# Kernel optimization log

Hardware: AMD Instinct MI355X
Metric: run time of the kernel (lower is better)

Reference implementation:

```python
import jax, jax.numpy as jnp
import numpy as np

B, N, C, P = 16, 4096, 4, 64
D = 128        # conv output channels (fixed in module)
WIN = 7        # window_size
ALPHA = 0.5
EPS = 1e-5     # BatchNorm eps


def setup_inputs() -> dict:
    key = jax.random.key(0)
    k1, k2, k3, k4 = jax.random.split(key, 4)
    x = jax.random.normal(k1, (B, N, C, P), jnp.float32)
    x_template = jax.random.normal(k2, (B, N, C, P), jnp.float32)
    # Conv1d(n_channel, 128, kernel_size=n_pts): weight [128, C, P], bias [128]
    W = jax.random.normal(k3, (D, C, P), jnp.float32) * 0.05
    b = jax.random.normal(k4, (D,), jnp.float32) * 0.01
    gamma = jnp.ones((D,), jnp.float32)   # BN weight init = 1
    beta = jnp.zeros((D,), jnp.float32)   # BN bias init = 0
    return {"x": x, "x_template": x_template, "W": W, "b": b, "gamma": gamma, "beta": beta}


def _embed(x_flat, W, b, gamma, beta):
    # Conv1d with kernel_size == full length -> contraction over (C, P), output length 1.
    h = jnp.einsum('ncp,dcp->nd', x_flat, W) + b           # [B*N, D]
    # BatchNorm1d in training mode: per-channel stats over the (B*N, L=1) batch.
    mean = h.mean(axis=0)
    var = h.var(axis=0)                                     # biased variance (torch BN)
    h = (h - mean) / jnp.sqrt(var + EPS) * gamma + beta
    return jnp.where(h >= 0, h, 0.1 * h)                    # LeakyReLU(0.1)


def reference(x, x_template, W, b, gamma, beta):
    nb, nc, ch, npt = x.shape
    hw = WIN // 2
    off = jnp.arange(-hw, hw + 1)
    raw = jnp.arange(nc)[:, None] + off[None, :]
    valid = (raw >= 0) & (raw < nc)                         # dedups clamped edge cols (matches dense mask)
    cols = jnp.clip(raw, 0, nc - 1)

    emb_x = _embed(x.reshape(nb * nc, ch, npt), W, b, gamma, beta).reshape(nb, nc, D)
    emb_t = _embed(x_template.reshape(nb * nc, ch, npt), W, b, gamma, beta).reshape(nb, nc, D)

    # Banded similarity: only the window entries the module actually uses.
    emb_t_win = emb_t[:, cols]
    sim = jnp.einsum('bnd,bnwd->bnw', emb_x, emb_t_win)

    # feat_fused = raw sim gathered at clamped window inds (duplicates at edges kept)
    feat_fused = sim

    # Masked softmax over the window (invalid = clamped duplicates excluded, as in dense mask)
    mx = jnp.where(valid, sim, -jnp.inf).max(axis=-1, keepdims=True)
    e = jnp.where(valid, jnp.exp(sim - mx), 0.0)
    attn = e / e.sum(axis=-1, keepdims=True)

    xt_flat = x_template.reshape(nb, nc, ch * npt)
    out = jnp.einsum('bnw,bnwe->bne', attn, xt_flat[:, cols])  # [B, N, C*P]
    out = out.reshape(nb, nc, ch, npt)
    out = ALPHA * x + (1.0 - ALPHA) * out
    return out, feat_fused
```

## Files before the change

### kernel.cpp

```cpp
#include <hip/hip_runtime.h>
#include <math.h>

#define BB 16
#define NN 4096
#define DD 128
#define KK 256
#define NROWS (BB*NN)
#define WIN 7
#define HWIN 3
#define ALPHA 0.5f
#define EPS 1e-5f

typedef __attribute__((ext_vector_type(8))) short bf16x8;
typedef __attribute__((ext_vector_type(4))) float f32x4;

__device__ __forceinline__ unsigned short f2b(float f) {
    unsigned u = __float_as_uint(f);
    u += 0x7FFFu + ((u >> 16) & 1u);
    return (unsigned short)(u >> 16);
}
__device__ __forceinline__ float b2f_lo(unsigned v) { return __uint_as_float(v << 16); }
__device__ __forceinline__ float b2f_hi(unsigned v) { return __uint_as_float(v & 0xFFFF0000u); }
__device__ __forceinline__ float lrelu(float v) { return v >= 0.f ? v : 0.1f * v; }

__device__ __forceinline__ uint4 pack8(float4 a, float4 b) {
    uint4 v;
    v.x = (unsigned)f2b(a.x)  | ((unsigned)f2b(a.y)  << 16);
    v.y = (unsigned)f2b(a.z)  | ((unsigned)f2b(a.w)  << 16);
    v.z = (unsigned)f2b(b.x)  | ((unsigned)f2b(b.y)  << 16);
    v.w = (unsigned)f2b(b.z)  | ((unsigned)f2b(b.w)  << 16);
    return v;
}

__global__ __launch_bounds__(256) void k_prep(
    const float* __restrict__ W, unsigned char* __restrict__ Wswz)
{
    const int id = blockIdx.x * 256 + threadIdx.x;
    const int d  = id >> 5, c8 = id & 31;
    const float4 a = *(const float4*)(&W[(size_t)d * KK + c8 * 8]);
    const float4 b = *(const float4*)(&W[(size_t)d * KK + c8 * 8 + 4]);
    const int off = d * 512 + ((c8 * 16) ^ ((d & 7) << 4));
    *(uint4*)(Wswz + off) = pack8(a, b);
}

__device__ __forceinline__ void stage_x(const float* __restrict__ X, int grow0,
                                        unsigned short* dst, int t)
{
    #pragma unroll
    for (int p = 0; p < 4; ++p) {
        const int j  = t + p * 512;
        const int r  = j >> 5, c8 = j & 31;
        const float* gp = X + (size_t)(grow0 + r) * KK + c8 * 8;
        const float4 a = *(const float4*)(gp);
        const float4 b = *(const float4*)(gp + 4);
        const int off = r * 512 + ((c8 * 16) ^ ((r & 7) << 4));
        *(uint4*)((char*)dst + off) = pack8(a, b);
    }
}

__global__ __launch_bounds__(512) void k_embed(
    const float* __restrict__ x,
    const float* __restrict__ xt,
    const uint4* __restrict__ Wswz,
    const float* __restrict__ bvec,
    unsigned short* __restrict__ h_out,
    float* __restrict__ sums)
{
    __shared__ unsigned short Wsh[128 * 256];
    __shared__ unsigned short Xs[2][64 * 256];

    const int blk  = blockIdx.x;
    const int src  = blk >> 7;
    const int tile = blk & 127;
    const int row0 = tile * 512;
    const float* __restrict__ X = src ? xt : x;
    unsigned short* __restrict__ H = h_out + (size_t)src * NROWS * DD;

    const int t    = threadIdx.x;
    const int lane = t & 63;
    const int w    = t >> 6;
    const int wm   = w & 1;
    const int wn   = w >> 1;
    const int l15  = lane & 15;
    const int lg   = lane >> 4;

    {
        uint4* d4 = (uint4*)Wsh;
        #pragma unroll
        for (int p = 0; p < 8; ++p) d4[t + p * 512] = Wswz[t + p * 512];
    }
    stage_x(X, row0, &Xs[0][0], t);
    __syncthreads();

    bf16x8 breg[2][8];
    #pragma unroll
    for (int n = 0; n < 2; ++n) {
        const int d = 32 * wn + 16 * n + l15;
        #pragma unroll
        for (int k = 0; k < 8; ++k) {
            const int addr = d * 512 + (((k * 64) + lg * 16) ^ ((d & 7) << 4));
            breg[n][k] = *(const bf16x8*)((const char*)Wsh + addr);
        }
    }

    const float bv0 = bvec[32 * wn + l15];
    const float bv1 = bvec[32 * wn + 16 + l15];
    float s0 = 0.f, s1 = 0.f, q0 = 0.f, q1 = 0.f;

    for (int st = 0; st < 8; ++st) {
        const int cur = st & 1;
        f32x4 acc[2][2];
        #pragma unroll
        for (int m = 0; m < 2; ++m)
            #pragma unroll
            for (int n = 0; n < 2; ++n)
                #pragma unroll
                for (int j = 0; j < 4; ++j) acc[m][n][j] = 0.f;

        const char* xb = (const char*)&Xs[cur][0];
        #pragma unroll
        for (int k = 0; k < 8; ++k) {
            bf16x8 af[2];
            #pragma unroll
            for (int m = 0; m < 2; ++m) {
                const int r = 32 * wm + 16 * m + l15;
                const int addr = r * 512 + (((k * 64) + lg * 16) ^ ((r & 7) << 4));
                af[m] = *(const bf16x8*)(xb + addr);
            }
            acc[0][0] = __builtin_amdgcn_mfma_f32_16x16x32_bf16(af[0], breg[0][k], acc[0][0], 0, 0, 0);
            acc[0][1] = __builtin_amdgcn_mfma_f32_16x16x32_bf16(af[0], breg[1][k], acc[0][1], 0, 0, 0);
            acc[1][0] = __builtin_amdgcn_mfma_f32_16x16x32_bf16(af[1], breg[0][k], acc[1][0], 0, 0, 0);
            acc[1][1] = __builtin_amdgcn_mfma_f32_16x16x32_bf16(af[1], breg[1][k], acc[1][1], 0, 0, 0);
        }

        if (st < 7) stage_x(X, row0 + (st + 1) * 64, &Xs[cur ^ 1][0], t);

        #pragma unroll
        for (int m = 0; m < 2; ++m) {
            #pragma unroll
            for (int j = 0; j < 4; ++j) {
                const int row = row0 + st * 64 + 32 * wm + 16 * m + lg * 4 + j;
                const float v0 = acc[m][0][j] + bv0;
                const float v1 = acc[m][1][j] + bv1;
                H[(size_t)row * DD + 32 * wn + l15]      = f2b(v0);
                H[(size_t)row * DD + 32 * wn + 16 + l15] = f2b(v1);
                s0 += v0; q0 += v0 * v0;
                s1 += v1; q1 += v1 * v1;
            }
        }
        __syncthreads();
    }

    s0 += __shfl_xor(s0, 16); s0 += __shfl_xor(s0, 32);
    s1 += __shfl_xor(s1, 16); s1 += __shfl_xor(s1, 32);
    q0 += __shfl_xor(q0, 16); q0 += __shfl_xor(q0, 32);
    q1 += __shfl_xor(q1, 16); q1 += __shfl_xor(q1, 32);
    float* red = (float*)Wsh;
    if (lane < 16) {
        red[(w * 2 + 0) * 16 + l15]       = s0;
        red[(w * 2 + 1) * 16 + l15]       = s1;
        red[256 + (w * 2 + 0) * 16 + l15] = q0;
        red[256 + (w * 2 + 1) * 16 + l15] = q1;
    }
    __syncthreads();
    if (t < 128) {
        const int wn_ = t >> 5, n_ = (t >> 4) & 1, li = t & 15;
        float S = 0.f, Q = 0.f;
        #pragma unroll
        for (int wm_ = 0; wm_ < 2; ++wm_) {
            const int w_ = wn_ * 2 + wm_;
            S += red[(w_ * 2 + n_) * 16 + li];
            Q += red[256 + (w_ * 2 + n_) * 16 + li];
        }
        atomicAdd(&sums[src * 256 + t], S);
        atomicAdd(&sums[src * 256 + 128 + t], Q);
    }
}

__global__ void k_stats(const float* __restrict__ sums,
                        const float* __restrict__ gamma,
                        const float* __restrict__ beta,
                        float* __restrict__ ss)
{
    const int t = threadIdx.x;
    if (t < 256) {
        const int src = t >> 7;
        const int d   = t & 127;
        const float invn = 1.0f / (float)NROWS;
        const float mean = sums[src * 256 + d] * invn;
        const float var  = sums[src * 256 + 128 + d] * invn - mean * mean;
        const float sc   = gamma[d] / sqrtf(var + EPS);
        const float sh   = beta[d] - mean * sc;
        ss[src * 256 + d]       = sc;
        ss[src * 256 + 128 + d] = sh;
    }
}

__global__ __launch_bounds__(256) void k_attn(
    const float* __restrict__ x,
    const float* __restrict__ xt,
    const unsigned short* __restrict__ h,
    const float* __restrict__ ss,
    float* __restrict__ out,
    float* __restrict__ feat)
{
    const int blk  = blockIdx.x;
    const int bb   = blk >> 7;
    const int tile = blk & 127;
    const int n0   = tile * 32;
    const int t    = threadIdx.x;

    __shared__ float ex[32][132];
    __shared__ float et[38][132];
    __shared__ float attnw[32][8];

    const unsigned short* __restrict__ Hx = h;
    const unsigned short* __restrict__ Ht = h + (size_t)NROWS * DD;
    const size_t rowbase = (size_t)bb * NN;

    #pragma unroll
    for (int p = 0; p < 2; ++p) {
        const int j = t + p * 256;
        const int r = j >> 4, c8 = j & 15;
        const uint4 u = *(const uint4*)(&Hx[(rowbase + n0 + r) * DD + c8 * 8]);
        const float4 sca = *(const float4*)(&ss[c8 * 8]);
        const float4 scb = *(const float4*)(&ss[c8 * 8 + 4]);
        const float4 sha = *(const float4*)(&ss[128 + c8 * 8]);
        const float4 shb = *(const float4*)(&ss[128 + c8 * 8 + 4]);
        float* dst = &ex[r][c8 * 8];
        dst[0] = lrelu(b2f_lo(u.x) * sca.x + sha.x);
        dst[1] = lrelu(b2f_hi(u.x) * sca.y + sha.y);
        dst[2] = lrelu(b2f_lo(u.y) * sca.z + sha.z);
        dst[3] = lrelu(b2f_hi(u.y) * sca.w + sha.w);
        dst[4] = lrelu(b2f_lo(u.z) * scb.x + shb.x);
        dst[5] = lrelu(b2f_hi(u.z) * scb.y + shb.y);
        dst[6] = lrelu(b2f_lo(u.w) * scb.z + shb.z);
        dst[7] = lrelu(b2f_hi(u.w) * scb.w + shb.w);
    }
    #pragma unroll
    for (int p = 0; p < 3; ++p) {
        const int j = t + p * 256;
        if (j < 608) {
            const int r = j >> 4, c8 = j & 15;
            int g = n0 - HWIN + r;
            g = min(max(g, 0), NN - 1);
            const uint4 u = *(const uint4*)(&Ht[(rowbase + g) * DD + c8 * 8]);
            const float4 sca = *(const float4*)(&ss[256 + c8 * 8]);
            const float4 scb = *(const float4*)(&ss[256 + c8 * 8 + 4]);
            const float4 sha = *(const float4*)(&ss[384 + c8 * 8]);
            const float4 shb = *(const float4*)(&ss[384 + c8 * 8 + 4]);
            float* dst = &et[r][c8 * 8];
            dst[0] = lrelu(b2f_lo(u.x) * sca.x + sha.x);
            dst[1] = lrelu(b2f_hi(u.x) * sca.y + sha.y);
            dst[2] = lrelu(b2f_lo(u.y) * sca.z + sha.z);
            dst[3] = lrelu(b2f_hi(u.y) * sca.w + sha.w);
            dst[4] = lrelu(b2f_lo(u.z) * scb.x + shb.x);
            dst[5] = lrelu(b2f_hi(u.z) * scb.y + shb.y);
            dst[6] = lrelu(b2f_lo(u.w) * scb.z + shb.z);
            dst[7] = lrelu(b2f_hi(u.w) * scb.w + shb.w);
        }
    }
    __syncthreads();

    if (t < 224) {
        const int n_i = t / 7;
        const int wv  = t % 7;
        const float* a = &ex[n_i][0];
        const float* b = &et[n_i + wv][0];
        float acc = 0.f;
        #pragma unroll
        for (int d4 = 0; d4 < 128; d4 += 4) {
            const float4 av = *(const float4*)(a + d4);
            const float4 bv = *(const float4*)(b + d4);
            acc += av.x * bv.x + av.y * bv.y + av.z * bv.z + av.w * bv.w;
        }
        feat[(rowbase + n0 + n_i) * WIN + wv] = acc;
        attnw[n_i][wv] = acc;
    }
    __syncthreads();

    unsigned short* xts = (unsigned short*)&et[0][0];
    if (t < 224) {
        #pragma unroll
        for (int p = 0; p < 6; ++p) {
            const int j = t + p * 224;
            if (j < 1216) {
                const int r = j >> 5, c8 = j & 31;
                int g = n0 - HWIN + r;
                g = min(max(g, 0), NN - 1);
                const float* gp = &xt[(rowbase + g) * KK + c8 * 8];
                const float4 a = *(const float4*)(gp);
                const float4 b = *(const float4*)(gp + 4);
                *(uint4*)((char*)xts + r * 512 + c8 * 16) = pack8(a, b);
            }
        }
    } else {
        const int n_i = t - 224;
        const int n = n0 + n_i;
        float mx = -1e30f;
        #pragma unroll
        for (int wv = 0; wv < WIN; ++wv) {
            const int c = n + wv - HWIN;
            if (c >= 0 && c < NN) mx = fmaxf(mx, attnw[n_i][wv]);
        }
        float e[WIN];
        float esum = 0.f;
        #pragma unroll
        for (int wv = 0; wv < WIN; ++wv) {
            const int c = n + wv - HWIN;
            const bool valid = (c >= 0 && c < NN);
            e[wv] = valid ? expf(attnw[n_i][wv] - mx) : 0.f;
            esum += e[wv];
        }
        const float inv = 1.0f / esum;
        #pragma unroll
        for (int wv = 0; wv < WIN; ++wv) attnw[n_i][wv] = e[wv] * inv;
    }
    __syncthreads();

    #pragma unroll
    for (int p = 0; p < 8; ++p) {
        const int idx = t + p * 256;
        const int n_i = idx >> 6, e4 = idx & 63;
        const int n = n0 + n_i;
        const float4 xv = *(const float4*)(&x[(rowbase + n) * KK + e4 * 4]);
        float4 acc = make_float4(0.f, 0.f, 0.f, 0.f);
        #pragma unroll
        for (int wv = 0; wv < WIN; ++wv) {
            const float aw = attnw[n_i][wv];
            const uint2 u = *(const uint2*)((const char*)xts + (n_i + wv) * 512 + e4 * 8);
            acc.x += aw * b2f_lo(u.x);
            acc.y += aw * b2f_hi(u.x);
            acc.z += aw * b2f_lo(u.y);
            acc.w += aw * b2f_hi(u.y);
        }
        float4 o;
        o.x = ALPHA * xv.x + (1.f - ALPHA) * acc.x;
        o.y = ALPHA * xv.y + (1.f - ALPHA) * acc.y;
        o.z = ALPHA * xv.z + (1.f - ALPHA) * acc.z;
        o.w = ALPHA * xv.w + (1.f - ALPHA) * acc.w;
        *(float4*)(&out[(rowbase + n) * KK + e4 * 4]) = o;
    }
}

extern "C" void kernel_launch(void* const* d_in, const int* in_sizes, int n_in,
                              void* d_out, int out_size, void* d_ws, size_t ws_size,
                              hipStream_t stream) {
    const float* x     = (const float*)d_in[0];
    const float* xt    = (const float*)d_in[1];
    const float* W     = (const float*)d_in[2];
    const float* bvec  = (const float*)d_in[3];
    const float* gamma = (const float*)d_in[4];
    const float* beta  = (const float*)d_in[5];

    float* out  = (float*)d_out;
    float* feat = out + (size_t)BB * NN * KK;

    char* ws = (char*)d_ws;
    unsigned short* h  = (unsigned short*)ws;
    float* sums        = (float*)(ws + 33554432);
    float* ss          = (float*)(ws + 33556480);
    unsigned char* Wsz = (unsigned char*)(ws + 33558528);

    hipMemsetAsync(sums, 0, 512 * sizeof(float), stream);
    k_prep<<<16, 256, 0, stream>>>(W, Wsz);
    k_embed<<<256, 512, 0, stream>>>(x, xt, (const uint4*)Wsz, bvec, h, sums);
    k_stats<<<1, 256, 0, stream>>>(sums, gamma, beta, ss);
    k_attn<<<2048, 256, 0, stream>>>(x, xt, h, ss, out, feat);
}
```

Baseline: 221.0 us.

## Drop W LDS staging, double embed grid, split load/write, fold stats into attn

k_prep now writes W already in per-lane MFMA fragment order, so k_embed loads B fragments straight from global and no longer holds 64KB of W in LDS. The smaller LDS footprint and launch_bounds(512,4) allow more resident blocks, and the grid doubles to 512 blocks of 256 rows each. X staging is split into a global load issued before the epilogue and an LDS write after it, which hides load latency. The separate k_stats launch is removed and every k_attn block recomputes scale and shift from the sums, trading a launch for a little redundant work.

```diff
diff --git a/kernel.cpp b/kernel.cpp
--- a/kernel.cpp
+++ b/kernel.cpp
@@ -33,46 +33,56 @@
 }
 
 __global__ __launch_bounds__(256) void k_prep(
-    const float* __restrict__ W, unsigned char* __restrict__ Wswz)
-{
-    const int id = blockIdx.x * 256 + threadIdx.x;
-    const int d  = id >> 5, c8 = id & 31;
-    const float4 a = *(const float4*)(&W[(size_t)d * KK + c8 * 8]);
-    const float4 b = *(const float4*)(&W[(size_t)d * KK + c8 * 8 + 4]);
-    const int off = d * 512 + ((c8 * 16) ^ ((d & 7) << 4));
-    *(uint4*)(Wswz + off) = pack8(a, b);
-}
-
-__device__ __forceinline__ void stage_x(const float* __restrict__ X, int grow0,
-                                        unsigned short* dst, int t)
+    const float* __restrict__ W, uint4* __restrict__ Wfrag)
+{
+    const int id   = blockIdx.x * 256 + threadIdx.x;
+    const int lane = id & 63, f = id >> 6;
+    const int k  = f & 7, n = (f >> 3) & 1, wn = f >> 4;
+    const int d  = 32 * wn + 16 * n + (lane & 15);
+    const int c  = k * 32 + (lane >> 4) * 8;
+    const float4 a = *(const float4*)(&W[(size_t)d * KK + c]);
+    const float4 b = *(const float4*)(&W[(size_t)d * KK + c + 4]);
+    Wfrag[id] = pack8(a, b);
+}
+
+__device__ __forceinline__ void stage_load(const float* __restrict__ X, int grow0,
+                                           int t, float4* ra, float4* rb)
 {
     #pragma unroll
     for (int p = 0; p < 4; ++p) {
-        const int j  = t + p * 512;
-        const int r  = j >> 5, c8 = j & 31;
+        const int j = t + p * 512;
+        const int r = j >> 5, c8 = j & 31;
         const float* gp = X + (size_t)(grow0 + r) * KK + c8 * 8;
-        const float4 a = *(const float4*)(gp);
-        const float4 b = *(const float4*)(gp + 4);
+        ra[p] = *(const float4*)(gp);
+        rb[p] = *(const float4*)(gp + 4);
+    }
+}
+__device__ __forceinline__ void stage_write(unsigned short* dst, int t,
+                                            const float4* ra, const float4* rb)
+{
+    #pragma unroll
+    for (int p = 0; p < 4; ++p) {
+        const int j = t + p * 512;
+        const int r = j >> 5, c8 = j & 31;
         const int off = r * 512 + ((c8 * 16) ^ ((r & 7) << 4));
-        *(uint4*)((char*)dst + off) = pack8(a, b);
-    }
-}
-
-__global__ __launch_bounds__(512) void k_embed(
+        *(uint4*)((char*)dst + off) = pack8(ra[p], rb[p]);
+    }
+}
+
+__global__ __launch_bounds__(512, 4) void k_embed(
     const float* __restrict__ x,
     const float* __restrict__ xt,
-    const uint4* __restrict__ Wswz,
+    const uint4* __restrict__ Wfrag,
     const float* __restrict__ bvec,
     unsigned short* __restrict__ h_out,
     float* __restrict__ sums)
 {
-    __shared__ unsigned short Wsh[128 * 256];
     __shared__ unsigned short Xs[2][64 * 256];
 
     const int blk  = blockIdx.x;
-    const int src  = blk >> 7;
-    const int tile = blk & 127;
-    const int row0 = tile * 512;
+    const int src  = blk >> 8;
+    const int tile = blk & 255;
+    const int row0 = tile * 256;
     const float* __restrict__ X = src ? xt : x;
     unsigned short* __restrict__ H = h_out + (size_t)src * NROWS * DD;
 
@@ -84,30 +94,25 @@
     const int l15  = lane & 15;
     const int lg   = lane >> 4;
 
-    {
-        uint4* d4 = (uint4*)Wsh;
-        #pragma unroll
-        for (int p = 0; p < 8; ++p) d4[t + p * 512] = Wswz[t + p * 512];
-    }
-    stage_x(X, row0, &Xs[0][0], t);
-    __syncthreads();
-
     bf16x8 breg[2][8];
     #pragma unroll
-    for (int n = 0; n < 2; ++n) {
-        const int d = 32 * wn + 16 * n + l15;
+    for (int n = 0; n < 2; ++n)
         #pragma unroll
         for (int k = 0; k < 8; ++k) {
-            const int addr = d * 512 + (((k * 64) + lg * 16) ^ ((d & 7) << 4));
-            breg[n][k] = *(const bf16x8*)((const char*)Wsh + addr);
-        }
-    }
+            uint4 u = Wfrag[((wn * 2 + n) * 8 + k) * 64 + lane];
+            breg[n][k] = *(bf16x8*)&u;
+        }
+
+    float4 ra[4], rb[4];
+    stage_load(X, row0, t, ra, rb);
+    stage_write(&Xs[0][0], t, ra, rb);
+    __syncthreads();
 
     const float bv0 = bvec[32 * wn + l15];
     const float bv1 = bvec[32 * wn + 16 + l15];
     float s0 = 0.f, s1 = 0.f, q0 = 0.f, q1 = 0.f;
 
-    for (int st = 0; st < 8; ++st) {
+    for (int st = 0; st < 4; ++st) {
         const int cur = st & 1;
         f32x4 acc[2][2];
         #pragma unroll
@@ -133,7 +138,7 @@
             acc[1][1] = __builtin_amdgcn_mfma_f32_16x16x32_bf16(af[1], breg[1][k], acc[1][1], 0, 0, 0);
         }
 
-        if (st < 7) stage_x(X, row0 + (st + 1) * 64, &Xs[cur ^ 1][0], t);
+        if (st < 3) stage_load(X, row0 + (st + 1) * 64, t, ra, rb);
 
         #pragma unroll
         for (int m = 0; m < 2; ++m) {
@@ -148,6 +153,8 @@
                 s1 += v1; q1 += v1 * v1;
             }
         }
+
+        if (st < 3) stage_write(&Xs[cur ^ 1][0], t, ra, rb);
         __syncthreads();
     }
 
@@ -155,7 +162,7 @@
     s1 += __shfl_xor(s1, 16); s1 += __shfl_xor(s1, 32);
     q0 += __shfl_xor(q0, 16); q0 += __shfl_xor(q0, 32);
     q1 += __shfl_xor(q1, 16); q1 += __shfl_xor(q1, 32);
-    float* red = (float*)Wsh;
+    float* red = (float*)&Xs[0][0];
     if (lane < 16) {
         red[(w * 2 + 0) * 16 + l15]       = s0;
         red[(w * 2 + 1) * 16 + l15]       = s1;
@@ -177,30 +184,13 @@
     }
 }
 
-__global__ void k_stats(const float* __restrict__ sums,
-                        const float* __restrict__ gamma,
-                        const float* __restrict__ beta,
-                        float* __restrict__ ss)
-{
-    const int t = threadIdx.x;
-    if (t < 256) {
-        const int src = t >> 7;
-        const int d   = t & 127;
-        const float invn = 1.0f / (float)NROWS;
-        const float mean = sums[src * 256 + d] * invn;
-        const float var  = sums[src * 256 + 128 + d] * invn - mean * mean;
-        const float sc   = gamma[d] / sqrtf(var + EPS);
-        const float sh   = beta[d] - mean * sc;
-        ss[src * 256 + d]       = sc;
-        ss[src * 256 + 128 + d] = sh;
-    }
-}
-
 __global__ __launch_bounds__(256) void k_attn(
     const float* __restrict__ x,
     const float* __restrict__ xt,
     const unsigned short* __restrict__ h,
-    const float* __restrict__ ss,
+    const float* __restrict__ sums,
+    const float* __restrict__ gamma,
+    const float* __restrict__ beta,
     float* __restrict__ out,
     float* __restrict__ feat)
 {
@@ -213,20 +203,32 @@
     __shared__ float ex[32][132];
     __shared__ float et[38][132];
     __shared__ float attnw[32][8];
+    __shared__ float ssl[512];
 
     const unsigned short* __restrict__ Hx = h;
     const unsigned short* __restrict__ Ht = h + (size_t)NROWS * DD;
     const size_t rowbase = (size_t)bb * NN;
+
+    {
+        const int s_ = t >> 7, d = t & 127;
+        const float invn = 1.0f / (float)NROWS;
+        const float mean = sums[s_ * 256 + d] * invn;
+        const float var  = sums[s_ * 256 + 128 + d] * invn - mean * mean;
+        const float sc   = gamma[d] / sqrtf(var + EPS);
+        ssl[s_ * 256 + d]       = sc;
+        ssl[s_ * 256 + 128 + d] = beta[d] - mean * sc;
+    }
+    __syncthreads();
 
     #pragma unroll
     for (int p = 0; p < 2; ++p) {
         const int j = t + p * 256;
         const int r = j >> 4, c8 = j & 15;
         const uint4 u = *(const uint4*)(&Hx[(rowbase + n0 + r) * DD + c8 * 8]);
-        const float4 sca = *(const float4*)(&ss[c8 * 8]);
-        const float4 scb = *(const float4*)(&ss[c8 * 8 + 4]);
-        const float4 sha = *(const float4*)(&ss[128 + c8 * 8]);
-        const float4 shb = *(const float4*)(&ss[128 + c8 * 8 + 4]);
+        const float4 sca = *(const float4*)(&ssl[c8 * 8]);
+        const float4 scb = *(const float4*)(&ssl[c8 * 8 + 4]);
+        const float4 sha = *(const float4*)(&ssl[128 + c8 * 8]);
+        const float4 shb = *(const float4*)(&ssl[128 + c8 * 8 + 4]);
         float* dst = &ex[r][c8 * 8];
         dst[0] = lrelu(b2f_lo(u.x) * sca.x + sha.x);
         dst[1] = lrelu(b2f_hi(u.x) * sca.y + sha.y);
@@ -245,10 +247,10 @@
             int g = n0 - HWIN + r;
             g = min(max(g, 0), NN - 1);
             const uint4 u = *(const uint4*)(&Ht[(rowbase + g) * DD + c8 * 8]);
-            const float4 sca = *(const float4*)(&ss[256 + c8 * 8]);
-            const float4 scb = *(const float4*)(&ss[256 + c8 * 8 + 4]);
-            const float4 sha = *(const float4*)(&ss[384 + c8 * 8]);
-            const float4 shb = *(const float4*)(&ss[384 + c8 * 8 + 4]);
+            const float4 sca = *(const float4*)(&ssl[256 + c8 * 8]);
+            const float4 scb = *(const float4*)(&ssl[256 + c8 * 8 + 4]);
+            const float4 sha = *(const float4*)(&ssl[384 + c8 * 8]);
+            const float4 shb = *(const float4*)(&ssl[384 + c8 * 8 + 4]);
             float* dst = &et[r][c8 * 8];
             dst[0] = lrelu(b2f_lo(u.x) * sca.x + sha.x);
             dst[1] = lrelu(b2f_hi(u.x) * sca.y + sha.y);
@@ -359,12 +361,10 @@
     char* ws = (char*)d_ws;
     unsigned short* h  = (unsigned short*)ws;
     float* sums        = (float*)(ws + 33554432);
-    float* ss          = (float*)(ws + 33556480);
-    unsigned char* Wsz = (unsigned char*)(ws + 33558528);
+    unsigned char* Wfr = (unsigned char*)(ws + 33556480);
 
     hipMemsetAsync(sums, 0, 512 * sizeof(float), stream);
-    k_prep<<<16, 256, 0, stream>>>(W, Wsz);
-    k_embed<<<256, 512, 0, stream>>>(x, xt, (const uint4*)Wsz, bvec, h, sums);
-    k_stats<<<1, 256, 0, stream>>>(sums, gamma, beta, ss);
-    k_attn<<<2048, 256, 0, stream>>>(x, xt, h, ss, out, feat);
-}
+    k_prep<<<16, 256, 0, stream>>>(W, (uint4*)Wfr);
+    k_embed<<<512, 512, 0, stream>>>(x, xt, (const uint4*)Wfr, bvec, h, sums);
+    k_attn<<<2048, 256, 0, stream>>>(x, xt, h, sums, gamma, beta, out, feat);
+}
```

After: 225.0 us. No clear change (+1.8%).
